# Kernel optimization log

Hardware: AMD Instinct MI355X
Metric: run time of the kernel (lower is better)

Reference implementation:

```python
import jax, jax.numpy as jnp
import numpy as np

N = 40000          # nodes
E = 640000         # directed edges (before self-loops)
NEG_SLOPE = 0.2    # PyG GATConv default negative_slope


def _segment_softmax(e, dst, n):
    # e: [E, H] per-edge logits, softmax over edges sharing the same dst
    m = jax.ops.segment_max(e, dst, num_segments=n)          # [n, H]
    ex = jnp.exp(e - m[dst])
    s = jax.ops.segment_sum(ex, dst, num_segments=n)         # [n, H]
    return ex / (s[dst] + 1e-16)


def _gat_layer(x, src, dst, W, att_src, att_dst, bias, heads, out_ch, concat, n):
    h = (x @ W).reshape(n, heads, out_ch)                    # [n, H, C]
    a_s = jnp.einsum('nhc,hc->nh', h, att_src)               # [n, H]
    a_d = jnp.einsum('nhc,hc->nh', h, att_dst)
    e = jax.nn.leaky_relu(a_s[src] + a_d[dst], NEG_SLOPE)    # [E, H]
    alpha = _segment_softmax(e, dst, n)                      # [E, H]
    msg = h[src] * alpha[:, :, None]                         # [E, H, C]
    out = jax.ops.segment_sum(msg, dst, num_segments=n)      # [n, H, C]
    out = out.reshape(n, heads * out_ch) if concat else out.mean(axis=1)
    return out + bias


def setup_inputs():
    key = jax.random.key(0)
    ks = jax.random.split(key, 12)
    x = jax.random.normal(ks[0], (N, 128), dtype=jnp.float32)
    edge_index = jax.random.randint(ks[1], (2, E), 0, N, dtype=jnp.int64)
    weights = jax.random.uniform(ks[2], (E,), dtype=jnp.float32)
    # GATConv(128, 64, heads=2)
    W1 = jax.random.normal(ks[3], (128, 2 * 64), dtype=jnp.float32) * 0.1
    att_src1 = jax.random.normal(ks[4], (2, 64), dtype=jnp.float32) * 0.1
    att_dst1 = jax.random.normal(ks[5], (2, 64), dtype=jnp.float32) * 0.1
    b1 = jnp.zeros((128,), dtype=jnp.float32)
    # GATConv(128, 4, heads=1, concat=False)
    W2 = jax.random.normal(ks[6], (128, 4), dtype=jnp.float32) * 0.1
    att_src2 = jax.random.normal(ks[7], (1, 4), dtype=jnp.float32) * 0.1
    att_dst2 = jax.random.normal(ks[8], (1, 4), dtype=jnp.float32) * 0.1
    b2 = jnp.zeros((4,), dtype=jnp.float32)
    return {'x': x, 'edge_index': edge_index, 'weights': weights,
            'W1': W1, 'att_src1': att_src1, 'att_dst1': att_dst1, 'b1': b1,
            'W2': W2, 'att_src2': att_src2, 'att_dst2': att_dst2, 'b2': b2}


def reference(x, edge_index, weights, W1, att_src1, att_dst1, b1, W2, att_src2, att_dst2, b2):
    # PyG default add_self_loops=True
    loop = jnp.arange(N, dtype=edge_index.dtype)
    src = jnp.concatenate([edge_index[0], loop])
    dst = jnp.concatenate([edge_index[1], loop])
    # dropout layers are identity in eval mode; `weights` unused (as in source)
    h = _gat_layer(x, src, dst, W1, att_src1, att_dst1, b1, 2, 64, True, N)
    h = jax.nn.elu(h)
    h = _gat_layer(h, src, dst, W2, att_src2, att_dst2, b2, 1, 4, False, N)
    return jax.nn.softmax(h, axis=1)
```

## Files before the change

kernel.cpp:

```cpp
#include <hip/hip_runtime.h>
#include <hip/hip_bf16.h>
#include <math.h>

#define N_NODES 40000
#define N_EDGES 640000
#define ET (N_EDGES + N_NODES)
#define SCAN_BLOCKS 40
#define SCAN_CHUNK 1000
#define G1_BLOCKS 1250
#define EPB 544

__device__ __forceinline__ float wave_red_sum(float v) {
#pragma unroll
  for (int m = 32; m >= 1; m >>= 1) v += __shfl_xor(v, m, 64);
  return v;
}
__device__ __forceinline__ int wave_red_sum_i(int v) {
#pragma unroll
  for (int m = 32; m >= 1; m >>= 1) v += __shfl_xor(v, m, 64);
  return v;
}
__device__ __forceinline__ float half_red_sum(float v) {
#pragma unroll
  for (int m = 16; m >= 1; m >>= 1) v += __shfl_xor(v, m, 64);
  return v;
}

__global__ __launch_bounds__(1024) void k_scanA(const int* __restrict__ deg,
                                                int* __restrict__ blocksum) {
  int t = threadIdx.x;
  int idx = blockIdx.x * SCAN_CHUNK + t;
  int v = (t < SCAN_CHUNK) ? deg[idx] : 0;
  int lane = t & 63, w = t >> 6;
  int s = wave_red_sum_i(v);
  __shared__ int ws[16];
  if (lane == 0) ws[w] = s;
  __syncthreads();
  if (t == 0) {
    int r = 0;
#pragma unroll
    for (int k = 0; k < 16; k++) r += ws[k];
    blocksum[blockIdx.x] = r;
  }
}

__global__ __launch_bounds__(1024) void k_scanB(const int* __restrict__ deg,
                                                const int* __restrict__ blocksum,
                                                int* __restrict__ off) {
  int t = threadIdx.x;
  int b = blockIdx.x;
  int lane = t & 63, w = t >> 6;
  __shared__ int carry_s;
  __shared__ int ws[16];
  if (w == 0) {
    int bs = (lane < b) ? blocksum[lane] : 0;
    int c = wave_red_sum_i(bs);
    if (lane == 0) carry_s = c;
  }
  int idx = b * SCAN_CHUNK + t;
  int v = (t < SCAN_CHUNK) ? deg[idx] : 0;
  int p = v;
#pragma unroll
  for (int o = 1; o < 64; o <<= 1) {
    int u = __shfl_up(p, o, 64);
    if (lane >= o) p += u;
  }
  if (lane == 63) ws[w] = p;
  __syncthreads();
  if (t == 0) {
    int r = 0;
#pragma unroll
    for (int k = 0; k < 16; k++) { int x = ws[k]; ws[k] = r; r += x; }
  }
  __syncthreads();
  int excl = carry_s + ws[w] + p - v;
  if (t < SCAN_CHUNK) off[idx] = excl;
  if (b == SCAN_BLOCKS - 1 && t == SCAN_CHUNK - 1) off[N_NODES] = excl + v;
}

__global__ void k_fill(const int* __restrict__ ei, const int* __restrict__ off,
                       const int* __restrict__ erank, int* __restrict__ csr_src) {
  int i = blockIdx.x * blockDim.x + threadIdx.x;
  if (i >= ET) return;
  int s, d;
  if (i < N_EDGES) { s = ei[i]; d = ei[N_EDGES + i]; }
  else             { s = d = i - N_EDGES; }
  csr_src[off[d] + erank[i]] = s;
}

__global__ __launch_bounds__(256) void k_gemm1(
    const float* __restrict__ x, const float* __restrict__ W1,
    const float* __restrict__ asv, const float* __restrict__ adv,
    const int* __restrict__ ei, int* __restrict__ deg, int* __restrict__ erank,
    __hip_bfloat16* __restrict__ h1b, float* __restrict__ a_s, float* __restrict__ a_d) {
  __shared__ float xs[32 * 128];
  int t = threadIdx.x;
  int n0 = blockIdx.x * 32;

  const float4* xg = (const float4*)(x + (size_t)n0 * 128);
  float4 xr0 = xg[t + 0 * 256];
  float4 xr1 = xg[t + 1 * 256];
  float4 xr2 = xg[t + 2 * 256];
  float4 xr3 = xg[t + 3 * 256];

  {
    int ebase = blockIdx.x * EPB;
#pragma unroll
    for (int r = 0; r < 2; r++) {
      int i = ebase + r * 256 + t;
      int d = (i < N_EDGES) ? ei[N_EDGES + i] : (i - N_EDGES);
      erank[i] = atomicAdd(&deg[d], 1);
    }
    if (t < EPB - 512) {
      int i = ebase + 512 + t;
      int d = (i < N_EDGES) ? ei[N_EDGES + i] : (i - N_EDGES);
      erank[i] = atomicAdd(&deg[d], 1);
    }
  }

  float4* xs4w = (float4*)xs;
  xs4w[t + 0 * 256] = xr0;
  xs4w[t + 1 * 256] = xr1;
  xs4w[t + 2 * 256] = xr2;
  xs4w[t + 3 * 256] = xr3;
  __syncthreads();

  int lane = t & 63;
  int g = t >> 6;
  int c0 = lane * 2;
  const float4* xs4 = (const float4*)(xs + (size_t)g * 8 * 128);

  float2 acc[8];
#pragma unroll
  for (int j = 0; j < 8; j++) acc[j] = make_float2(0.f, 0.f);

  float2 w0 = *(const float2*)(W1 + (size_t)0 * 128 + c0);
  float2 w1 = *(const float2*)(W1 + (size_t)1 * 128 + c0);
  float2 w2 = *(const float2*)(W1 + (size_t)2 * 128 + c0);
  float2 w3 = *(const float2*)(W1 + (size_t)3 * 128 + c0);

  for (int k4 = 0; k4 < 32; k4++) {
    float2 nw0, nw1, nw2, nw3;
    if (k4 < 31) {
      nw0 = *(const float2*)(W1 + (size_t)(4 * k4 + 4) * 128 + c0);
      nw1 = *(const float2*)(W1 + (size_t)(4 * k4 + 5) * 128 + c0);
      nw2 = *(const float2*)(W1 + (size_t)(4 * k4 + 6) * 128 + c0);
      nw3 = *(const float2*)(W1 + (size_t)(4 * k4 + 7) * 128 + c0);
    }
#pragma unroll
    for (int j = 0; j < 8; j++) {
      float4 xv = xs4[j * 32 + k4];
      acc[j].x = fmaf(xv.x, w0.x, acc[j].x);
      acc[j].y = fmaf(xv.x, w0.y, acc[j].y);
      acc[j].x = fmaf(xv.y, w1.x, acc[j].x);
      acc[j].y = fmaf(xv.y, w1.y, acc[j].y);
      acc[j].x = fmaf(xv.z, w2.x, acc[j].x);
      acc[j].y = fmaf(xv.z, w2.y, acc[j].y);
      acc[j].x = fmaf(xv.w, w3.x, acc[j].x);
      acc[j].y = fmaf(xv.w, w3.y, acc[j].y);
    }
    w0 = nw0; w1 = nw1; w2 = nw2; w3 = nw3;
  }

  float2 av_s = *(const float2*)(asv + c0);
  float2 av_d = *(const float2*)(adv + c0);
  int head = lane >> 5;
#pragma unroll
  for (int j = 0; j < 8; j++) {
    int n = n0 + g * 8 + j;
    __hip_bfloat162 hv;
    hv.x = __float2bfloat16(acc[j].x);
    hv.y = __float2bfloat16(acc[j].y);
    *(__hip_bfloat162*)(h1b + (size_t)n * 128 + c0) = hv;
    float rs = half_red_sum(acc[j].x * av_s.x + acc[j].y * av_s.y);
    float rd = half_red_sum(acc[j].x * av_d.x + acc[j].y * av_d.y);
    if ((lane & 31) == 0) {
      a_s[n * 2 + head] = rs;
      a_d[n * 2 + head] = rd;
    }
  }
}

__global__ __launch_bounds__(256) void k_agg1(
    const int* __restrict__ off, const int* __restrict__ csr_src,
    const float* __restrict__ a_s, const float* __restrict__ a_d,
    const __hip_bfloat16* __restrict__ h1b, const float* __restrict__ b1,
    const float* __restrict__ W2, const float* __restrict__ as2,
    const float* __restrict__ ad2,
    float* __restrict__ h2pack, float* __restrict__ a_d2) {
  int wv = threadIdx.x >> 6;
  int v = blockIdx.x * 4 + wv;
  int lane = threadIdx.x & 63;
  int head = lane >> 5;
  int beg = off[v], end = off[v + 1];
  float2 Ad = *(const float2*)(a_d + 2 * v);
  const __hip_bfloat162* h1b2 = (const __hip_bfloat162*)h1b;

  __shared__ int    lds_s[4][64];
  __shared__ float2 lds_e[4][64];

  float acc0 = 0.f, acc1 = 0.f;
  float sum0 = 0.f, sum1 = 0.f;
  for (int base = beg; base < end; base += 64) {
    int idx = base + lane;
    int sreg = 0;
    float ex0 = 0.f, ex1 = 0.f;
    if (idx < end) {
      sreg = csr_src[idx];
      float2 As = *(const float2*)(a_s + 2 * sreg);
      float e0 = As.x + Ad.x; e0 = (e0 >= 0.f) ? e0 : 0.2f * e0;
      float e1 = As.y + Ad.y; e1 = (e1 >= 0.f) ? e1 : 0.2f * e1;
      ex0 = __expf(e0); ex1 = __expf(e1);
    }
    sum0 += ex0; sum1 += ex1;
    lds_s[wv][lane] = sreg;
    lds_e[wv][lane] = make_float2(ex0, ex1);
    __threadfence_block();

    int jmax = min(64, end - base);
    int j = 0;
    for (; j + 4 <= jmax; j += 4) {
      int sA = lds_s[wv][j + 0];
      int sB = lds_s[wv][j + 1];
      int sC = lds_s[wv][j + 2];
      int sD = lds_s[wv][j + 3];
      float2 wA = lds_e[wv][j + 0];
      float2 wB = lds_e[wv][j + 1];
      float2 wC = lds_e[wv][j + 2];
      float2 wD = lds_e[wv][j + 3];
      __hip_bfloat162 hA = h1b2[(size_t)sA * 64 + lane];
      __hip_bfloat162 hB = h1b2[(size_t)sB * 64 + lane];
      __hip_bfloat162 hC = h1b2[(size_t)sC * 64 + lane];
      __hip_bfloat162 hD = h1b2[(size_t)sD * 64 + lane];
      float eA = head ? wA.y : wA.x;
      float eB = head ? wB.y : wB.x;
      float eC = head ? wC.y : wC.x;
      float eD = head ? wD.y : wD.x;
      acc0 = fmaf(eA, __bfloat162float(hA.x), acc0);
      acc1 = fmaf(eA, __bfloat162float(hA.y), acc1);
      acc0 = fmaf(eB, __bfloat162float(hB.x), acc0);
      acc1 = fmaf(eB, __bfloat162float(hB.y), acc1);
      acc0 = fmaf(eC, __bfloat162float(hC.x), acc0);
      acc1 = fmaf(eC, __bfloat162float(hC.y), acc1);
      acc0 = fmaf(eD, __bfloat162float(hD.x), acc0);
      acc1 = fmaf(eD, __bfloat162float(hD.y), acc1);
    }
    for (; j < jmax; j++) {
      int s = lds_s[wv][j];
      float2 wv2 = lds_e[wv][j];
      float ex = head ? wv2.y : wv2.x;
      __hip_bfloat162 hv = h1b2[(size_t)s * 64 + lane];
      acc0 = fmaf(ex, __bfloat162float(hv.x), acc0);
      acc1 = fmaf(ex, __bfloat162float(hv.y), acc1);
    }
    __threadfence_block();
  }
  sum0 = wave_red_sum(sum0);
  sum1 = wave_red_sum(sum1);
  float inv = 1.f / ((head ? sum1 : sum0) + 1e-16f);

  float2 bv = *(const float2*)(b1 + 2 * lane);
  float o0 = acc0 * inv + bv.x;
  float o1 = acc1 * inv + bv.y;
  o0 = (o0 > 0.f) ? o0 : expm1f(o0);
  o1 = (o1 > 0.f) ? o1 : expm1f(o1);

  float4 wA = *(const float4*)(W2 + (2 * lane) * 4);
  float4 wB = *(const float4*)(W2 + (2 * lane + 1) * 4);
  float p0 = wave_red_sum(o0 * wA.x + o1 * wB.x);
  float p1 = wave_red_sum(o0 * wA.y + o1 * wB.y);
  float p2 = wave_red_sum(o0 * wA.z + o1 * wB.z);
  float p3 = wave_red_sum(o0 * wA.w + o1 * wB.w);
  if (lane == 0) {
    float4 q = {p0, p1, p2, p3};
    *(float4*)(h2pack + (size_t)v * 8) = q;
    h2pack[(size_t)v * 8 + 4] =
        p0 * as2[0] + p1 * as2[1] + p2 * as2[2] + p3 * as2[3];
    a_d2[v] = p0 * ad2[0] + p1 * ad2[1] + p2 * ad2[2] + p3 * ad2[3];
  }
}

__global__ __launch_bounds__(256) void k_agg2(
    const int* __restrict__ off, const int* __restrict__ csr_src,
    const float* __restrict__ h2pack, const float* __restrict__ a_d,
    const float* __restrict__ b2, float* __restrict__ out) {
  int v = blockIdx.x * 4 + (threadIdx.x >> 6);
  int lane = threadIdx.x & 63;
  int beg = off[v], end = off[v + 1];
  float adv = a_d[v];
  const float4* pk = (const float4*)h2pack;

  float sum = 0.f;
  float4 acc = {0.f, 0.f, 0.f, 0.f};
  for (int i = beg + lane; i < end; i += 64) {
    int s = csr_src[i];
    float4 r0 = pk[2 * s];
    float4 r1 = pk[2 * s + 1];
    float e = r1.x + adv;
    e = (e >= 0.f) ? e : 0.2f * e;
    float ex = __expf(e);
    sum += ex;
    acc.x = fmaf(ex, r0.x, acc.x);
    acc.y = fmaf(ex, r0.y, acc.y);
    acc.z = fmaf(ex, r0.z, acc.z);
    acc.w = fmaf(ex, r0.w, acc.w);
  }
  sum = wave_red_sum(sum);
  acc.x = wave_red_sum(acc.x);
  acc.y = wave_red_sum(acc.y);
  acc.z = wave_red_sum(acc.z);
  acc.w = wave_red_sum(acc.w);

  if (lane == 0) {
    float invd = 1.f / (sum + 1e-16f);
    float o0 = acc.x * invd + b2[0];
    float o1 = acc.y * invd + b2[1];
    float o2 = acc.z * invd + b2[2];
    float o3 = acc.w * invd + b2[3];
    float mx = fmaxf(fmaxf(o0, o1), fmaxf(o2, o3));
    float e0 = __expf(o0 - mx), e1 = __expf(o1 - mx);
    float e2 = __expf(o2 - mx), e3 = __expf(o3 - mx);
    float s4 = e0 + e1 + e2 + e3;
    float4 r = {e0 / s4, e1 / s4, e2 / s4, e3 / s4};
    *(float4*)(out + (size_t)v * 4) = r;
  }
}

extern "C" void kernel_launch(void* const* d_in, const int* in_sizes, int n_in,
                              void* d_out, int out_size, void* d_ws, size_t ws_size,
                              hipStream_t stream) {
  const float* x   = (const float*)d_in[0];
  const int*   ei  = (const int*)d_in[1];
  const float* W1  = (const float*)d_in[3];
  const float* as1 = (const float*)d_in[4];
  const float* ad1 = (const float*)d_in[5];
  const float* b1  = (const float*)d_in[6];
  const float* W2  = (const float*)d_in[7];
  const float* as2 = (const float*)d_in[8];
  const float* ad2 = (const float*)d_in[9];
  const float* b2  = (const float*)d_in[10];
  float* out = (float*)d_out;

  char* w = (char*)d_ws;
  auto alloc = [&](size_t bytes) {
    char* p = w;
    w += (bytes + 255) & ~(size_t)255;
    return p;
  };
  int*   deg     = (int*)alloc((size_t)N_NODES * 4);
  int*   off     = (int*)alloc((size_t)(N_NODES + 1) * 4);
  int*   erank   = (int*)alloc((size_t)ET * 4);
  int*   csr_src = (int*)alloc((size_t)ET * 4);
  int*   blocksum= (int*)alloc((size_t)SCAN_BLOCKS * 4);
  __hip_bfloat16* h1b = (__hip_bfloat16*)alloc((size_t)N_NODES * 128 * 2);
  float* a_s1w   = (float*)alloc((size_t)N_NODES * 2 * 4);
  float* a_d1w   = (float*)alloc((size_t)N_NODES * 2 * 4);
  float* h2pack  = (float*)alloc((size_t)N_NODES * 8 * 4);
  float* a_d2w   = (float*)alloc((size_t)N_NODES * 4);

  hipMemsetAsync(deg, 0, (size_t)N_NODES * 4, stream);
  k_gemm1<<<G1_BLOCKS, 256, 0, stream>>>(x, W1, as1, ad1, ei, deg, erank,
                                         h1b, a_s1w, a_d1w);
  k_scanA<<<SCAN_BLOCKS, 1024, 0, stream>>>(deg, blocksum);
  k_scanB<<<SCAN_BLOCKS, 1024, 0, stream>>>(deg, blocksum, off);
  k_fill<<<(ET + 255) / 256, 256, 0, stream>>>(ei, off, erank, csr_src);

  k_agg1<<<N_NODES / 4, 256, 0, stream>>>(off, csr_src, a_s1w, a_d1w, h1b, b1,
                                          W2, as2, ad2, h2pack, a_d2w);
  k_agg2<<<N_NODES / 4, 256, 0, stream>>>(off, csr_src, h2pack, a_d2w, b2, out);
}
```

Measured before the change: 201.2 us.

## Split edge histogram out of GEMM kernel and use 16-lane groups in agg2

Moves the degree histogram and edge-rank atomics out of the first GEMM into a separate k_hist kernel, and runs the GEMM after the CSR build. This undoes an earlier fusion that hid atomic latency behind the x loads. It also changes layer-2 aggregation to give each node 16 lanes instead of a full 64-lane wave, since average degree is about 17. That avoids mostly idle lanes and shortens the reductions. The cost is one extra kernel launch and the loss of overlap between the atomics and the GEMM.

```diff
diff --git a/kernel.cpp b/kernel.cpp
--- a/kernel.cpp
+++ b/kernel.cpp
@@ -7,8 +7,6 @@
 #define ET (N_EDGES + N_NODES)
 #define SCAN_BLOCKS 40
 #define SCAN_CHUNK 1000
-#define G1_BLOCKS 1250
-#define EPB 544
 
 __device__ __forceinline__ float wave_red_sum(float v) {
 #pragma unroll
@@ -24,6 +22,19 @@
 #pragma unroll
   for (int m = 16; m >= 1; m >>= 1) v += __shfl_xor(v, m, 64);
   return v;
+}
+__device__ __forceinline__ float red16(float v) {
+#pragma unroll
+  for (int m = 8; m >= 1; m >>= 1) v += __shfl_xor(v, m, 64);
+  return v;
+}
+
+__global__ void k_hist(const int* __restrict__ ei, int* __restrict__ deg,
+                       int* __restrict__ erank) {
+  int i = blockIdx.x * blockDim.x + threadIdx.x;
+  if (i >= ET) return;
+  int d = (i < N_EDGES) ? ei[N_EDGES + i] : (i - N_EDGES);
+  erank[i] = atomicAdd(&deg[d], 1);
 }
 
 __global__ __launch_bounds__(1024) void k_scanA(const int* __restrict__ deg,
@@ -91,38 +102,16 @@
 __global__ __launch_bounds__(256) void k_gemm1(
     const float* __restrict__ x, const float* __restrict__ W1,
     const float* __restrict__ asv, const float* __restrict__ adv,
-    const int* __restrict__ ei, int* __restrict__ deg, int* __restrict__ erank,
     __hip_bfloat16* __restrict__ h1b, float* __restrict__ a_s, float* __restrict__ a_d) {
   __shared__ float xs[32 * 128];
   int t = threadIdx.x;
   int n0 = blockIdx.x * 32;
-
-  const float4* xg = (const float4*)(x + (size_t)n0 * 128);
-  float4 xr0 = xg[t + 0 * 256];
-  float4 xr1 = xg[t + 1 * 256];
-  float4 xr2 = xg[t + 2 * 256];
-  float4 xr3 = xg[t + 3 * 256];
-
   {
-    int ebase = blockIdx.x * EPB;
-#pragma unroll
-    for (int r = 0; r < 2; r++) {
-      int i = ebase + r * 256 + t;
-      int d = (i < N_EDGES) ? ei[N_EDGES + i] : (i - N_EDGES);
-      erank[i] = atomicAdd(&deg[d], 1);
-    }
-    if (t < EPB - 512) {
-      int i = ebase + 512 + t;
-      int d = (i < N_EDGES) ? ei[N_EDGES + i] : (i - N_EDGES);
-      erank[i] = atomicAdd(&deg[d], 1);
-    }
-  }
-
-  float4* xs4w = (float4*)xs;
-  xs4w[t + 0 * 256] = xr0;
-  xs4w[t + 1 * 256] = xr1;
-  xs4w[t + 2 * 256] = xr2;
-  xs4w[t + 3 * 256] = xr3;
+    const float4* xg = (const float4*)(x + (size_t)n0 * 128);
+    float4* xs4 = (float4*)xs;
+#pragma unroll
+    for (int i = 0; i < 4; i++) xs4[t + i * 256] = xg[t + i * 256];
+  }
   __syncthreads();
 
   int lane = t & 63;
@@ -284,15 +273,16 @@
     const int* __restrict__ off, const int* __restrict__ csr_src,
     const float* __restrict__ h2pack, const float* __restrict__ a_d,
     const float* __restrict__ b2, float* __restrict__ out) {
-  int v = blockIdx.x * 4 + (threadIdx.x >> 6);
-  int lane = threadIdx.x & 63;
+  int t = threadIdx.x;
+  int grp = t >> 4, gl = t & 15;
+  int v = blockIdx.x * 16 + grp;
   int beg = off[v], end = off[v + 1];
   float adv = a_d[v];
   const float4* pk = (const float4*)h2pack;
 
   float sum = 0.f;
   float4 acc = {0.f, 0.f, 0.f, 0.f};
-  for (int i = beg + lane; i < end; i += 64) {
+  for (int i = beg + gl; i < end; i += 16) {
     int s = csr_src[i];
     float4 r0 = pk[2 * s];
     float4 r1 = pk[2 * s + 1];
@@ -305,13 +295,13 @@
     acc.z = fmaf(ex, r0.z, acc.z);
     acc.w = fmaf(ex, r0.w, acc.w);
   }
-  sum = wave_red_sum(sum);
-  acc.x = wave_red_sum(acc.x);
-  acc.y = wave_red_sum(acc.y);
-  acc.z = wave_red_sum(acc.z);
-  acc.w = wave_red_sum(acc.w);
-
-  if (lane == 0) {
+  sum = red16(sum);
+  acc.x = red16(acc.x);
+  acc.y = red16(acc.y);
+  acc.z = red16(acc.z);
+  acc.w = red16(acc.w);
+
+  if (gl == 0) {
     float invd = 1.f / (sum + 1e-16f);
     float o0 = acc.x * invd + b2[0];
     float o1 = acc.y * invd + b2[1];
@@ -359,13 +349,13 @@
   float* a_d2w   = (float*)alloc((size_t)N_NODES * 4);
 
   hipMemsetAsync(deg, 0, (size_t)N_NODES * 4, stream);
-  k_gemm1<<<G1_BLOCKS, 256, 0, stream>>>(x, W1, as1, ad1, ei, deg, erank,
-                                         h1b, a_s1w, a_d1w);
+  k_hist<<<(ET + 255) / 256, 256, 0, stream>>>(ei, deg, erank);
   k_scanA<<<SCAN_BLOCKS, 1024, 0, stream>>>(deg, blocksum);
   k_scanB<<<SCAN_BLOCKS, 1024, 0, stream>>>(deg, blocksum, off);
   k_fill<<<(ET + 255) / 256, 256, 0, stream>>>(ei, off, erank, csr_src);
 
+  k_gemm1<<<N_NODES / 32, 256, 0, stream>>>(x, W1, as1, ad1, h1b, a_s1w, a_d1w);
   k_agg1<<<N_NODES / 4, 256, 0, stream>>>(off, csr_src, a_s1w, a_d1w, h1b, b1,
                                           W2, as2, ad2, h2pack, a_d2w);
-  k_agg2<<<N_NODES / 4, 256, 0, stream>>>(off, csr_src, h2pack, a_d2w, b2, out);
-}
+  k_agg2<<<N_NODES / 16, 256, 0, stream>>>(off, csr_src, h2pack, a_d2w, b2, out);
+}
```

New measurement: 195.7 us. 2.7% less time.
